# Kernel optimization log

Hardware: AMD Instinct MI355X
Metric: run time of the kernel (lower is better)

## Reference

```python
import jax, jax.numpy as jnp
import numpy as np

LMBDA = {"rec": 1.0, "bpp": 1.0}


def setup_inputs() -> dict:
    key = jax.random.key(0)
    k1, k2, k3 = jax.random.split(key, 3)
    B, P, D = 8, 4096, 3
    x_hat = jax.random.normal(k1, (B, P, D), dtype=jnp.float32)
    pos = jax.random.normal(k2, (B, P, D), dtype=jnp.float32)
    # latent likelihoods in (0, 1], CompressAI-style [B, C, L]
    likelihoods = jax.random.uniform(k3, (B, 192, 1024), dtype=jnp.float32,
                                     minval=1e-6, maxval=1.0)
    return {"x_hat": x_hat, "pos": pos, "likelihoods": likelihoods}


def chamfer_distance(x, y):
    # x: [B, P, 3], y: [B, Q, 3]; squared-distance chamfer, mean over points,
    # summed both directions, averaged over batch (pytorch3d default 'mean').
    x2 = jnp.sum(x * x, axis=-1)                       # [B, P]
    y2 = jnp.sum(y * y, axis=-1)                       # [B, Q]
    xy = jnp.einsum("bpd,bqd->bpq", x, y)              # [B, P, Q]
    d2 = x2[:, :, None] + y2[:, None, :] - 2.0 * xy    # [B, P, Q]
    d2 = jnp.maximum(d2, 0.0)
    cham_x = jnp.mean(jnp.min(d2, axis=2), axis=1)     # [B] x -> y NN
    cham_y = jnp.mean(jnp.min(d2, axis=1), axis=1)     # [B] y -> x NN
    return jnp.mean(cham_x + cham_y)


def reference(x_hat, pos, likelihoods):
    B, P, _ = pos.shape
    # rate loss: bits per point over the whole batch
    num_points = B * P
    bpp_loss = jnp.sum(-jnp.log2(likelihoods)) / num_points
    # reconstruction loss: bidirectional chamfer distance
    rec_loss = chamfer_distance(x_hat, pos)
    loss = LMBDA["rec"] * rec_loss + LMBDA["bpp"] * bpp_loss
    return loss, bpp_loss, rec_loss
```

## Files before the change

kernel.cpp:

```cpp
#include <hip/hip_runtime.h>
#include <math.h>

#define BATCH   8
#define NPTS    4096
#define THREADS 512
#define WAVES   8
#define ROWS_PB 128
#define CHUNK   512
#define NSTEP   4
#define NBLOCKS 512

#define LIK_F4      393216
#define LIK_PER_BLK (LIK_F4 / NBLOCKS)

typedef __attribute__((ext_vector_type(8)))  __bf16 bf16x8;
typedef __attribute__((ext_vector_type(16))) float  f32x16;

__device__ inline bf16x8 packFeat(float f0, float f1, float f2, float f3, float f4) {
    bf16x8 r;
    r[0] = (__bf16)f0; r[1] = (__bf16)f1; r[2] = (__bf16)f2;
    r[3] = (__bf16)f3; r[4] = (__bf16)f4;
    r[5] = (__bf16)0.0f; r[6] = (__bf16)0.0f; r[7] = (__bf16)0.0f;
    return r;
}

__global__ __launch_bounds__(THREADS, 2) void fused_kernel(
    const float* __restrict__ Xin, const float* __restrict__ Yin,
    const float* __restrict__ lik,
    float* __restrict__ recPartial, float* __restrict__ bppPartial)
{
    const float* X; const float* Y;
    if (blockIdx.z == 0) { X = Xin; Y = Yin; }
    else                 { X = Yin; Y = Xin; }

    const int b = blockIdx.y;
    const int rowBase = (int)blockIdx.x * ROWS_PB;
    const int blk = ((int)blockIdx.z * gridDim.y + blockIdx.y) * gridDim.x + blockIdx.x;

    const int tid  = threadIdx.x;
    const int lane = tid & 63;
    const int w    = tid >> 6;
    const int rg   = w >> 1;
    const int ph   = w & 1;
    const int li   = lane & 31;
    const int hi   = lane >> 5;

    __shared__ bf16x8 yfeat[2][2][CHUNK];
    __shared__ float  cmb[2][ROWS_PB];
    __shared__ float  wr[WAVES], wb[WAVES];

    float bs = 0.0f;
    {
        const float4* l4 = (const float4*)lik + (size_t)blk * LIK_PER_BLK;
        for (int i = tid; i < LIK_PER_BLK; i += THREADS) {
            float4 v = l4[i];
            bs -= __log2f(v.x * v.y * v.z * v.w);
        }
    }

    bf16x8 a;
    {
        const float* p = X + ((size_t)b * NPTS + rowBase + rg * 32 + li) * 3;
        float x0 = p[0], x1 = p[1], x2 = p[2];
        a = packFeat(x0, x1, x2, fmaf(x0, x0, fmaf(x1, x1, x2 * x2)), 1.0f);
    }

    f32x16 m, kZero;
    #pragma unroll
    for (int j = 0; j < 16; ++j) { m[j] = 3.0e38f; kZero[j] = 0.0f; }

    const int sh = tid >> 8;
    const int sc = tid & 255;

    {
        const float* p0 = Y + ((size_t)b * NPTS + sh * 2048 + sc) * 3;
        float u0 = p0[0], u1 = p0[1], u2 = p0[2];
        const float* p1 = p0 + 256 * 3;
        float v0 = p1[0], v1 = p1[1], v2 = p1[2];
        yfeat[0][sh][sc]       = packFeat(-2.f*u0, -2.f*u1, -2.f*u2, 1.0f,
                                          fmaf(u0,u0,fmaf(u1,u1,u2*u2)));
        yfeat[0][sh][sc + 256] = packFeat(-2.f*v0, -2.f*v1, -2.f*v2, 1.0f,
                                          fmaf(v0,v0,fmaf(v1,v1,v2*v2)));
    }
    __syncthreads();

    int buf = 0;
    for (int s = 0; s < NSTEP; ++s) {
        float u0, u1, u2, v0, v1, v2;
        if (s + 1 < NSTEP) {
            const float* p0 = Y + ((size_t)b * NPTS + sh * 2048 + (s + 1) * CHUNK + sc) * 3;
            u0 = p0[0]; u1 = p0[1]; u2 = p0[2];
            const float* p1 = p0 + 256 * 3;
            v0 = p1[0]; v1 = p1[1]; v2 = p1[2];
        }

        const bf16x8* yb = &yfeat[buf][ph][0];
        #pragma unroll 2
        for (int f = 0; f < 16; f += 2) {
            bf16x8 bA = yb[f * 32 + li];
            bf16x8 bB = yb[(f + 1) * 32 + li];
            f32x16 d = __builtin_amdgcn_mfma_f32_32x32x16_bf16(a, bA, kZero, 0, 0, 0);
            f32x16 e = __builtin_amdgcn_mfma_f32_32x32x16_bf16(a, bB, kZero, 0, 0, 0);
            #pragma unroll
            for (int j = 0; j < 16; ++j)
                m[j] = fminf(fminf(d[j], e[j]), m[j]);
        }

        if (s + 1 < NSTEP) {
            yfeat[buf ^ 1][sh][sc]       = packFeat(-2.f*u0, -2.f*u1, -2.f*u2, 1.0f,
                                                    fmaf(u0,u0,fmaf(u1,u1,u2*u2)));
            yfeat[buf ^ 1][sh][sc + 256] = packFeat(-2.f*v0, -2.f*v1, -2.f*v2, 1.0f,
                                                    fmaf(v0,v0,fmaf(v1,v1,v2*v2)));
        }
        __syncthreads();
        buf ^= 1;
    }

    #pragma unroll
    for (int mask = 1; mask <= 16; mask <<= 1)
        #pragma unroll
        for (int j = 0; j < 16; ++j)
            m[j] = fminf(m[j], __shfl_xor(m[j], mask, 64));

    if (li == 0) {
        #pragma unroll
        for (int j = 0; j < 16; ++j) {
            int ri = (j & 3) + 8 * (j >> 2) + 4 * hi;
            cmb[ph][rg * 32 + ri] = m[j];
        }
    }
    __syncthreads();

    float s = 0.0f;
    if (tid < ROWS_PB) {
        float mv = fminf(cmb[0][tid], cmb[1][tid]);
        s = fmaxf(0.5f * mv, 0.0f);
    }
    #pragma unroll
    for (int off = 32; off >= 1; off >>= 1) {
        s  += __shfl_down(s, off, 64);
        bs += __shfl_down(bs, off, 64);
    }
    if (lane == 0) { wr[w] = s; wb[w] = bs; }
    __syncthreads();
    if (tid == 0) {
        float rs = 0.0f, bb = 0.0f;
        #pragma unroll
        for (int j = 0; j < WAVES; ++j) { rs += wr[j]; bb += wb[j]; }
        recPartial[blk] = rs;
        bppPartial[blk] = bb;
    }
}

__global__ __launch_bounds__(256) void final_kernel(const float* __restrict__ recPartial,
                                                    const float* __restrict__ bppPartial,
                                                    float* __restrict__ out) {
    float sr = 0.0f, sb = 0.0f;
    for (int i = threadIdx.x; i < NBLOCKS; i += 256) {
        sr += recPartial[i];
        sb += bppPartial[i];
    }
    #pragma unroll
    for (int off = 32; off >= 1; off >>= 1) {
        sr += __shfl_down(sr, off, 64);
        sb += __shfl_down(sb, off, 64);
    }
    __shared__ float wrf[4], wbf[4];
    int lane = threadIdx.x & 63, w = threadIdx.x >> 6;
    if (lane == 0) { wrf[w] = sr; wbf[w] = sb; }
    __syncthreads();
    if (threadIdx.x == 0) {
        float rec = (wrf[0] + wrf[1] + wrf[2] + wrf[3]) * (1.0f / 32768.0f);
        float bpp = (wbf[0] + wbf[1] + wbf[2] + wbf[3]) * (1.0f / 32768.0f);
        out[0] = rec + bpp;
        out[1] = bpp;
        out[2] = rec;
    }
}

extern "C" void kernel_launch(void* const* d_in, const int* in_sizes, int n_in,
                              void* d_out, int out_size, void* d_ws, size_t ws_size,
                              hipStream_t stream) {
    const float* x_hat = (const float*)d_in[0];
    const float* pos   = (const float*)d_in[1];
    const float* lik   = (const float*)d_in[2];
    float* out = (float*)d_out;

    float* recPartial = (float*)d_ws;
    float* bppPartial = recPartial + NBLOCKS;

    dim3 grid(NPTS / ROWS_PB, BATCH, 2);
    fused_kernel<<<grid, THREADS, 0, stream>>>(x_hat, pos, lik, recPartial, bppPartial);
    final_kernel<<<1, 256, 0, stream>>>(recPartial, bppPartial, out);
}
```

Before: 20.03 us.

## Precompute bf16 point features and bpp sum in a separate prep kernel

```diff
diff --git a/kernel.cpp b/kernel.cpp
--- a/kernel.cpp
+++ b/kernel.cpp
@@ -10,8 +10,9 @@
 #define NSTEP   4
 #define NBLOCKS 512
 
-#define LIK_F4      393216
-#define LIK_PER_BLK (LIK_F4 / NBLOCKS)
+#define NPT_TOT 32768
+#define NBPP    512
+#define LIK_PER_BLK 768
 
 typedef __attribute__((ext_vector_type(8)))  __bf16 bf16x8;
 typedef __attribute__((ext_vector_type(16))) float  f32x16;
@@ -24,18 +25,51 @@
     return r;
 }
 
+__global__ __launch_bounds__(256) void prep_kernel(
+    const float* __restrict__ x_hat, const float* __restrict__ pos,
+    const float* __restrict__ lik,
+    bf16x8* __restrict__ feat, float* __restrict__ bppPartial)
+{
+    const int blk = blockIdx.x;
+    if (blk < 256) {
+        int g = blk * 256 + threadIdx.x;
+        int input = g >> 15, pt = g & (NPT_TOT - 1);
+        const float* p = (input ? pos : x_hat) + (size_t)pt * 3;
+        float x0 = p[0], x1 = p[1], x2 = p[2];
+        float n = fmaf(x0, x0, fmaf(x1, x1, x2 * x2));
+        feat[input * NPT_TOT + pt]           = packFeat(x0, x1, x2, n, 1.0f);
+        feat[2 * NPT_TOT + input * NPT_TOT + pt] =
+            packFeat(-2.f * x0, -2.f * x1, -2.f * x2, 1.0f, n);
+    } else {
+        int bb = blk - 256;
+        const float4* l4 = (const float4*)lik + (size_t)bb * LIK_PER_BLK;
+        float bs = 0.0f;
+        for (int i = threadIdx.x; i < LIK_PER_BLK; i += 256) {
+            float4 v = l4[i];
+            bs -= __log2f(v.x * v.y * v.z * v.w);
+        }
+        #pragma unroll
+        for (int off = 32; off >= 1; off >>= 1) bs += __shfl_down(bs, off, 64);
+        __shared__ float wsum[4];
+        int lane = threadIdx.x & 63, w = threadIdx.x >> 6;
+        if (lane == 0) wsum[w] = bs;
+        __syncthreads();
+        if (threadIdx.x == 0)
+            bppPartial[bb] = wsum[0] + wsum[1] + wsum[2] + wsum[3];
+    }
+}
+
 __global__ __launch_bounds__(THREADS, 2) void fused_kernel(
-    const float* __restrict__ Xin, const float* __restrict__ Yin,
-    const float* __restrict__ lik,
-    float* __restrict__ recPartial, float* __restrict__ bppPartial)
+    const bf16x8* __restrict__ feat, float* __restrict__ recPartial)
 {
-    const float* X; const float* Y;
-    if (blockIdx.z == 0) { X = Xin; Y = Yin; }
-    else                 { X = Yin; Y = Xin; }
+    const int z = blockIdx.z;
+    const bf16x8* rowF = feat + (z ? NPT_TOT : 0);
+    const bf16x8* colF = feat + 2 * NPT_TOT + (z ? 0 : NPT_TOT);
 
     const int b = blockIdx.y;
     const int rowBase = (int)blockIdx.x * ROWS_PB;
-    const int blk = ((int)blockIdx.z * gridDim.y + blockIdx.y) * gridDim.x + blockIdx.x;
+    const int blk = (z * gridDim.y + b) * gridDim.x + blockIdx.x;
+    const size_t colBase = (size_t)b * NPTS;
 
     const int tid  = threadIdx.x;
     const int lane = tid & 63;
@@ -45,56 +79,33 @@
     const int li   = lane & 31;
     const int hi   = lane >> 5;
 
-    __shared__ bf16x8 yfeat[2][2][CHUNK];
+    __shared__ bf16x8 yfeat[2][2 * CHUNK];
     __shared__ float  cmb[2][ROWS_PB];
-    __shared__ float  wr[WAVES], wb[WAVES];
-
-    float bs = 0.0f;
+    __shared__ float  wr[WAVES];
+
+    bf16x8 a = rowF[colBase + rowBase + rg * 32 + li];
+
+    f32x16 m, kZero;
+    #pragma unroll
+    for (int j = 0; j < 16; ++j) { m[j] = 3.0e38f; kZero[j] = 0.0f; }
+
     {
-        const float4* l4 = (const float4*)lik + (size_t)blk * LIK_PER_BLK;
-        for (int i = tid; i < LIK_PER_BLK; i += THREADS) {
-            float4 v = l4[i];
-            bs -= __log2f(v.x * v.y * v.z * v.w);
-        }
-    }
-
-    bf16x8 a;
-    {
-        const float* p = X + ((size_t)b * NPTS + rowBase + rg * 32 + li) * 3;
-        float x0 = p[0], x1 = p[1], x2 = p[2];
-        a = packFeat(x0, x1, x2, fmaf(x0, x0, fmaf(x1, x1, x2 * x2)), 1.0f);
-    }
-
-    f32x16 m, kZero;
-    #pragma unroll
-    for (int j = 0; j < 16; ++j) { m[j] = 3.0e38f; kZero[j] = 0.0f; }
-
-    const int sh = tid >> 8;
-    const int sc = tid & 255;
-
-    {
-        const float* p0 = Y + ((size_t)b * NPTS + sh * 2048 + sc) * 3;
-        float u0 = p0[0], u1 = p0[1], u2 = p0[2];
-        const float* p1 = p0 + 256 * 3;
-        float v0 = p1[0], v1 = p1[1], v2 = p1[2];
-        yfeat[0][sh][sc]       = packFeat(-2.f*u0, -2.f*u1, -2.f*u2, 1.0f,
-                                          fmaf(u0,u0,fmaf(u1,u1,u2*u2)));
-        yfeat[0][sh][sc + 256] = packFeat(-2.f*v0, -2.f*v1, -2.f*v2, 1.0f,
-                                          fmaf(v0,v0,fmaf(v1,v1,v2*v2)));
+        bf16x8 v1 = colF[colBase + tid];
+        bf16x8 v2 = colF[colBase + 2048 + tid];
+        yfeat[0][tid]       = v1;
+        yfeat[0][tid + 512] = v2;
     }
     __syncthreads();
 
     int buf = 0;
     for (int s = 0; s < NSTEP; ++s) {
-        float u0, u1, u2, v0, v1, v2;
+        bf16x8 n1, n2;
         if (s + 1 < NSTEP) {
-            const float* p0 = Y + ((size_t)b * NPTS + sh * 2048 + (s + 1) * CHUNK + sc) * 3;
-            u0 = p0[0]; u1 = p0[1]; u2 = p0[2];
-            const float* p1 = p0 + 256 * 3;
-            v0 = p1[0]; v1 = p1[1]; v2 = p1[2];
-        }
-
-        const bf16x8* yb = &yfeat[buf][ph][0];
+            n1 = colF[colBase + (s + 1) * CHUNK + tid];
+            n2 = colF[colBase + 2048 + (s + 1) * CHUNK + tid];
+        }
+
+        const bf16x8* yb = &yfeat[buf][ph * CHUNK];
         #pragma unroll 2
         for (int f = 0; f < 16; f += 2) {
             bf16x8 bA = yb[f * 32 + li];
@@ -107,10 +118,8 @@
         }
 
         if (s + 1 < NSTEP) {
-            yfeat[buf ^ 1][sh][sc]       = packFeat(-2.f*u0, -2.f*u1, -2.f*u2, 1.0f,
-                                                    fmaf(u0,u0,fmaf(u1,u1,u2*u2)));
-            yfeat[buf ^ 1][sh][sc + 256] = packFeat(-2.f*v0, -2.f*v1, -2.f*v2, 1.0f,
-                                                    fmaf(v0,v0,fmaf(v1,v1,v2*v2)));
+            yfeat[buf ^ 1][tid]       = n1;
+            yfeat[buf ^ 1][tid + 512] = n2;
         }
         __syncthreads();
         buf ^= 1;
@@ -137,18 +146,14 @@
         s = fmaxf(0.5f * mv, 0.0f);
     }
     #pragma unroll
-    for (int off = 32; off >= 1; off >>= 1) {
-        s  += __shfl_down(s, off, 64);
-        bs += __shfl_down(bs, off, 64);
-    }
-    if (lane == 0) { wr[w] = s; wb[w] = bs; }
+    for (int off = 32; off >= 1; off >>= 1) s += __shfl_down(s, off, 64);
+    if (lane == 0) wr[w] = s;
     __syncthreads();
     if (tid == 0) {
-        float rs = 0.0f, bb = 0.0f;
-        #pragma unroll
-        for (int j = 0; j < WAVES; ++j) { rs += wr[j]; bb += wb[j]; }
+        float rs = 0.0f;
+        #pragma unroll
+        for (int j = 0; j < WAVES; ++j) rs += wr[j];
         recPartial[blk] = rs;
-        bppPartial[blk] = bb;
     }
 }
 
@@ -156,10 +161,8 @@
                                                     const float* __restrict__ bppPartial,
                                                     float* __restrict__ out) {
     float sr = 0.0f, sb = 0.0f;
-    for (int i = threadIdx.x; i < NBLOCKS; i += 256) {
-        sr += recPartial[i];
-        sb += bppPartial[i];
-    }
+    for (int i = threadIdx.x; i < NBLOCKS; i += 256) sr += recPartial[i];
+    for (int i = threadIdx.x; i < NBPP;    i += 256) sb += bppPartial[i];
     #pragma unroll
     for (int off = 32; off >= 1; off >>= 1) {
         sr += __shfl_down(sr, off, 64);
@@ -186,10 +189,14 @@
     const float* lik   = (const float*)d_in[2];
     float* out = (float*)d_out;
 
-    float* recPartial = (float*)d_ws;
+    bf16x8* feat = (bf16x8*)d_ws;
+    float* recPartial = (float*)((char*)d_ws + 4 * (size_t)NPT_TOT * sizeof(bf16x8));
     float* bppPartial = recPartial + NBLOCKS;
 
+    prep_kernel<<<768, 256, 0, stream>>>(x_hat, pos, lik, feat, bppPartial);
+
     dim3 grid(NPTS / ROWS_PB, BATCH, 2);
-    fused_kernel<<<grid, THREADS, 0, stream>>>(x_hat, pos, lik, recPartial, bppPartial);
+    fused_kernel<<<grid, THREADS, 0, stream>>>(feat, recPartial);
+
     final_kernel<<<1, 256, 0, stream>>>(recPartial, bppPartial, out);
 }
```

New measurement: 25.02 us. 1.25x slower.
